# Kernel optimization log

Hardware: AMD Instinct MI355X
Metric: run time of the kernel (lower is better)

## Reference

```python
import jax, jax.numpy as jnp
import numpy as np

B, S, D, H = 2, 4096, 512, 8
HD = D // H
SCALE = float(np.sqrt(HD))


def setup_inputs() -> dict:
    key = jax.random.key(0)
    ks = jax.random.split(key, 11)
    std = 1.0 / np.sqrt(D)
    inp = {
        "query": jax.random.normal(ks[0], (B, S, D), jnp.float32),
        "key": jax.random.normal(ks[1], (B, S, D), jnp.float32),
        "value": jax.random.normal(ks[2], (B, S, D), jnp.float32),
        "Wq": jax.random.normal(ks[3], (D, D), jnp.float32) * std,
        "bq": jnp.zeros((D,), jnp.float32),
        "Wk": jax.random.normal(ks[4], (D, D), jnp.float32) * std,
        "bk": jnp.zeros((D,), jnp.float32),
        "Wv": jax.random.normal(ks[5], (D, D), jnp.float32) * std,
        "bv": jnp.zeros((D,), jnp.float32),
        "Wo": jax.random.normal(ks[6], (D, D), jnp.float32) * std,
        "bo": jnp.zeros((D,), jnp.float32),
    }
    return inp


def reference(query, key, value, Wq, bq, Wk, bk, Wv, bv, Wo, bo):
    # Linear projections, split into heads: [B, H, S, HD]
    def proj(x, W, b):
        y = jnp.einsum('bsd,df->bsf', x, W) + b
        return y.reshape(B, -1, H, HD).transpose(0, 2, 1, 3)

    Q = proj(query, Wq, bq)
    K = proj(key, Wk, bk)
    V = proj(value, Wv, bv)

    # Full [B, H, S, S] score matrix (faithful to the naive original)
    scores = jnp.einsum('bhqd,bhkd->bhqk', Q, K) / SCALE
    attn = jax.nn.softmax(scores, axis=-1)  # dropout = identity in eval
    attended = jnp.einsum('bhqk,bhkd->bhqd', attn, V)
    attended = attended.transpose(0, 2, 1, 3).reshape(B, -1, D)
    return jnp.einsum('bsd,df->bsf', attended, Wo) + bo
```

## Files before the change

kernel.cpp:

```cpp
#include <hip/hip_runtime.h>

typedef short short8 __attribute__((ext_vector_type(8)));
typedef short short4v __attribute__((ext_vector_type(4)));
typedef float f32x4 __attribute__((ext_vector_type(4)));
typedef float f32x16 __attribute__((ext_vector_type(16)));
typedef unsigned uint2v __attribute__((ext_vector_type(2)));

typedef __attribute__((address_space(1))) void gvoid;
typedef __attribute__((address_space(3))) void lvoid;

#define DEV static __device__ __forceinline__

constexpr int Dm = 512;
constexpr int Sm = 4096;
constexpr int Hh = 8;
constexpr long NTe = (long)2 * Sm * Dm;

#define QSCALE 0.18033688011112042f

DEV short f2bf(float f) {
  union { float f; unsigned u; } v; v.f = f;
  unsigned r = v.u + 0x7FFFu + ((v.u >> 16) & 1u);
  return (short)(r >> 16);
}

DEV float bf2f(short s) {
  unsigned u = ((unsigned)(unsigned short)s) << 16;
  union { unsigned u; float f; } v; v.u = u;
  return v.f;
}

DEV float exp2_fast(float x) {
#if __has_builtin(__builtin_amdgcn_exp2f)
  return __builtin_amdgcn_exp2f(x);
#else
  return exp2f(x);
#endif
}

DEV float max3f(float a, float b, float c) { return fmaxf(fmaxf(a, b), c); }

DEV unsigned cvt_pk_bf16(float lo, float hi) {
  unsigned r;
  asm("v_cvt_pk_bf16_f32 %0, %1, %2" : "=v"(r) : "v"(lo), "v"(hi));
  return r;
}

DEV int fr(int r) { return (r & 7) ^ (((r >> 3) & 1) << 2); }

DEV uint2v pl32swap(unsigned a, unsigned b) {
  return __builtin_amdgcn_permlane32_swap(a, b, false, false);
}
DEV float swap_max(float x) { return fmaxf(x, __shfl_xor(x, 32, 64)); }
DEV float swap_add(float x) { return x + __shfl_xor(x, 32, 64); }

DEV void async16(const void* g, void* l) {
  __builtin_amdgcn_global_load_lds((gvoid*)g, (lvoid*)l, 16, 0, 0);
}

__global__ __launch_bounds__(256) void cast_qkv(
    const float* __restrict__ q, const float* __restrict__ k,
    const float* __restrict__ v, short* __restrict__ xq,
    short* __restrict__ xk, short* __restrict__ xv) {
  int t = blockIdx.y;
  const float* src = (t == 0) ? q : (t == 1) ? k : v;
  short* dst = (t == 0) ? xq : (t == 1) ? xk : xv;
  long i = (long)(blockIdx.x * 256 + threadIdx.x) * 4;
  float4 f = *(const float4*)(src + i);
  short4v o;
  o[0] = f2bf(f.x); o[1] = f2bf(f.y); o[2] = f2bf(f.z); o[3] = f2bf(f.w);
  *(short4v*)(dst + i) = o;
}

__global__ __launch_bounds__(256) void wtrans(
    const float* __restrict__ wq, const float* __restrict__ wk,
    const float* __restrict__ wv, const float* __restrict__ wo,
    short* __restrict__ wt) {
  __shared__ short T[64 * 72];
  const int tid = threadIdx.x;
  const int n0 = blockIdx.x * 64, k0 = blockIdx.y * 64, w = blockIdx.z;
  const float* W = (w == 0) ? wq : (w == 1) ? wk : (w == 2) ? wv : wo;
  for (int t = 0; t < 4; ++t) {
    int flat = t * 256 + tid;
    int r = flat >> 4, c4 = flat & 15;
    float4 f = *(const float4*)(W + (k0 + r) * 512 + n0 + c4 * 4);
    T[(c4 * 4 + 0) * 72 + r] = f2bf(f.x);
    T[(c4 * 4 + 1) * 72 + r] = f2bf(f.y);
    T[(c4 * 4 + 2) * 72 + r] = f2bf(f.z);
    T[(c4 * 4 + 3) * 72 + r] = f2bf(f.w);
  }
  __syncthreads();
  for (int t = 0; t < 2; ++t) {
    int flat = t * 256 + tid;
    int r = flat >> 3, c = flat & 7;
    short8 v = *(const short8*)(T + r * 72 + c * 8);
    *(short8*)(wt + ((long)w << 18) + (n0 + r) * 512 + k0 + c * 8) = v;
  }
}

__global__ __launch_bounds__(256) void vtrans(
    const short* __restrict__ V, short* __restrict__ VT) {
  __shared__ short T[64 * 72];
  const int tid = threadIdx.x;
  const int s0 = blockIdx.x * 64, d0 = blockIdx.y * 64, b = blockIdx.z;
  for (int t = 0; t < 2; ++t) {
    int flat = t * 256 + tid;
    int sl = flat >> 3, c = flat & 7;
    short8 v = *(const short8*)(V + ((long)b * Sm + s0 + sl) * Dm + d0 + c * 8);
    for (int j = 0; j < 8; ++j) T[(c * 8 + j) * 72 + sl] = v[j];
  }
  __syncthreads();
  for (int t = 0; t < 2; ++t) {
    int flat = t * 256 + tid;
    int dl = flat >> 3, c = flat & 7;
    short8 v = *(const short8*)(T + dl * 72 + c * 8);
    *(short8*)(VT + ((long)b * Dm + d0 + dl) * Sm + s0 + c * 8) = v;
  }
}

template <bool OUT_BF16>
DEV void gemm_body(const short* __restrict__ A, const short* __restrict__ Bt,
                   const float* __restrict__ bias, float scale,
                   void* __restrict__ Yv, short* As, short* Bs) {
  constexpr int K = 512, N = 512, BK = 64;
  const int tid = threadIdx.x, lane = tid & 63, w = tid >> 6;
  const int lm = lane & 15, lg = lane >> 4;
  const int wr = w >> 1, wc = w & 1;
  const long bm = (long)blockIdx.y * 128;
  const long bn = (long)blockIdx.x * 128;
  f32x4 zero = {0.f, 0.f, 0.f, 0.f};
  f32x4 acc[4][4];
  for (int m = 0; m < 4; ++m)
    for (int n = 0; n < 4; ++n) acc[m][n] = zero;
  for (int k0 = 0; k0 < K; k0 += BK) {
    __syncthreads();
    for (int t = 0; t < 4; ++t) {
      int flat = t * 256 + tid;
      int row = flat >> 3, c = flat & 7;
      async16(A + (bm + row) * K + k0 + ((c ^ fr(row)) * 8), As + flat * 8);
    }
    for (int t = 0; t < 4; ++t) {
      int flat = t * 256 + tid;
      int row = flat >> 3, c = flat & 7;
      async16(Bt + (bn + row) * K + k0 + ((c ^ fr(row)) * 8), Bs + flat * 8);
    }
    __syncthreads();
    for (int kk = 0; kk < 2; ++kk) {
      short8 a[4], b[4];
      for (int m = 0; m < 4; ++m)
        a[m] = *(const short8*)(As + (wr * 64 + m * 16 + lm) * BK +
                                ((kk * 4 + lg) ^ fr(lm)) * 8);
      for (int n = 0; n < 4; ++n)
        b[n] = *(const short8*)(Bs + (wc * 64 + n * 16 + lm) * BK +
                                ((kk * 4 + lg) ^ fr(lm)) * 8);
      for (int m = 0; m < 4; ++m)
        for (int n = 0; n < 4; ++n)
          acc[m][n] = __builtin_amdgcn_mfma_f32_16x16x32_bf16(a[m], b[n], acc[m][n], 0, 0, 0);
    }
  }
  for (int m = 0; m < 4; ++m)
    for (int n = 0; n < 4; ++n) {
      long row0 = bm + wr * 64 + m * 16 + lg * 4;
      int col = (int)bn + wc * 64 + n * 16 + lm;
      float bb = bias[col];
      for (int j = 0; j < 4; ++j) {
        float val = (acc[m][n][j] + bb) * scale;
        if (OUT_BF16)
          ((short*)Yv)[(row0 + j) * N + col] = f2bf(val);
        else
          ((float*)Yv)[(row0 + j) * N + col] = val;
      }
    }
}

__global__ __launch_bounds__(256) void gemm_proj(
    const short* __restrict__ Xq, const short* __restrict__ Xk,
    const short* __restrict__ Xv, const short* __restrict__ Wt,
    const float* __restrict__ bq, const float* __restrict__ bk,
    const float* __restrict__ bv, short* __restrict__ Qb,
    short* __restrict__ Kb, short* __restrict__ Vb) {
  __shared__ short As[128 * 64];
  __shared__ short Bs[128 * 64];
  int z = blockIdx.z;
  const short* A = (z == 0) ? Xq : (z == 1) ? Xk : Xv;
  const short* Bt = Wt + (long)z * 512 * 512;
  const float* bias = (z == 0) ? bq : (z == 1) ? bk : bv;
  short* Y = (z == 0) ? Qb : (z == 1) ? Kb : Vb;
  float scale = (z == 0) ? QSCALE : 1.f;
  gemm_body<true>(A, Bt, bias, scale, Y, As, Bs);
}

__global__ __launch_bounds__(256) void gemm_out(
    const short* __restrict__ A, const short* __restrict__ Bt,
    const float* __restrict__ bias, float* __restrict__ Y) {
  __shared__ short As[128 * 64];
  __shared__ short Bs[128 * 64];
  gemm_body<false>(A, Bt, bias, 1.f, Y, As, Bs);
}

template <int NSPLIT>
__global__ __launch_bounds__(512) void attn(
    const short* __restrict__ Qb, const short* __restrict__ Kb,
    const short* __restrict__ VTb, short* __restrict__ Op0,
    short* __restrict__ OpRest, float2* __restrict__ Ml) {
  __shared__ short Ks[4][64 * 64];
  __shared__ short Vt[4][64 * 64];
  const int tid = threadIdx.x, lane = tid & 63, w = tid >> 6;
  const int q32 = lane & 31, l5 = lane >> 5;
  const int bh = blockIdx.y, b = bh >> 3, h = bh & 7;
  const int z = blockIdx.z;
  constexpr int KVLEN = Sm / NSPLIT;
  const int kvbase = z * KVLEN;
  const long baseQ = (long)b * Sm * Dm + h * 64;
  const long baseVT = ((long)b * Dm + h * 64) * Sm;
  const int q0w = blockIdx.x * 256 + w * 32;

  short8 qf[4];
#pragma unroll
  for (int ks = 0; ks < 4; ++ks)
    qf[ks] = *(const short8*)(Qb + baseQ + (long)(q0w + q32) * Dm + ks * 16 + l5 * 8);

  f32x16 o0, o1;
#pragma unroll
  for (int r = 0; r < 16; ++r) { o0[r] = 0.f; o1[r] = 0.f; }
  float mrun = -1e30f, lrun = 0.f;

  const int r0 = tid >> 3, c0 = tid & 7;
  const short* gk0 = Kb + baseQ + (long)(kvbase + r0) * Dm + (c0 ^ fr(r0)) * 8;
  const short* gv0 = VTb + baseVT + (long)r0 * Sm + kvbase + (c0 ^ fr(r0)) * 8;
  const int l0 = tid * 8;

  auto stage = [&](int buf) {
    async16(gk0, &Ks[buf][l0]);
    async16(gv0, &Vt[buf][l0]);
    gk0 += 64 * Dm; gv0 += 64;
  };

  stage(0);
  stage(1);
  __syncthreads();

  const int cxor = fr(q32);

  auto tile_body = [&](int buf) {
    f32x16 sc0, sc1;
#pragma unroll
    for (int r = 0; r < 16; ++r) { sc0[r] = 0.f; sc1[r] = 0.f; }
    __builtin_amdgcn_s_setprio(1);
#pragma unroll
    for (int ks = 0; ks < 4; ++ks) {
      int cx = (2 * ks + l5) ^ cxor;
      short8 kf0 = *(const short8*)(&Ks[buf][q32 * 64 + cx * 8]);
      short8 kf1 = *(const short8*)(&Ks[buf][(32 + q32) * 64 + cx * 8]);
      sc0 = __builtin_amdgcn_mfma_f32_32x32x16_bf16(kf0, qf[ks], sc0, 0, 0, 0);
      sc1 = __builtin_amdgcn_mfma_f32_32x32x16_bf16(kf1, qf[ks], sc1, 0, 0, 0);
    }
    __builtin_amdgcn_s_setprio(0);

    float t1 = max3f(sc0[0], sc0[1], sc0[2]);
    float t2 = max3f(sc0[3], sc0[4], sc0[5]);
    float t3 = max3f(sc0[6], sc0[7], sc0[8]);
    float t4 = max3f(sc0[9], sc0[10], sc0[11]);
    float t5 = max3f(sc0[12], sc0[13], sc0[14]);
    float ma = max3f(max3f(t1, t2, t3), max3f(t4, t5, sc0[15]), sc1[0]);
    t1 = max3f(sc1[1], sc1[2], sc1[3]);
    t2 = max3f(sc1[4], sc1[5], sc1[6]);
    t3 = max3f(sc1[7], sc1[8], sc1[9]);
    t4 = max3f(sc1[10], sc1[11], sc1[12]);
    t5 = max3f(sc1[13], sc1[14], sc1[15]);
    float tmax_lane = fmaxf(ma, max3f(max3f(t1, t2, t3), t4, t5));

    if (__any(tmax_lane > mrun + 8.f)) {
      float tmax = swap_max(tmax_lane);
      float mi = fmaxf(mrun, tmax);
      float cc = exp2_fast(mrun - mi);
      mrun = mi;
      lrun *= cc;
#pragma unroll
      for (int r = 0; r < 16; ++r) {
        float ccr = __shfl(cc, ((r & 3) + 8 * (r >> 2)) + 4 * l5, 32);
        o0[r] *= ccr;
        o1[r] *= ccr;
      }
    }

    float la[4] = {0.f, 0.f, 0.f, 0.f}, lb[4] = {0.f, 0.f, 0.f, 0.f};
#pragma unroll
    for (int r = 0; r < 16; ++r) {
      sc0[r] = exp2_fast(sc0[r] - mrun); la[r & 3] += sc0[r];
      sc1[r] = exp2_fast(sc1[r] - mrun); lb[r & 3] += sc1[r];
    }
    lrun += ((la[0] + la[1]) + (la[2] + la[3])) +
            ((lb[0] + lb[1]) + (lb[2] + lb[3]));

    __builtin_amdgcn_s_setprio(1);
#pragma unroll
    for (int kc = 0; kc < 4; ++kc) {
      const f32x16& sch = (kc < 2) ? sc0 : sc1;
      const int bb = 8 * (kc & 1);
      unsigned A = cvt_pk_bf16(sch[bb + 0], sch[bb + 1]);
      unsigned B = cvt_pk_bf16(sch[bb + 2], sch[bb + 3]);
      unsigned C = cvt_pk_bf16(sch[bb + 4], sch[bb + 5]);
      unsigned D = cvt_pk_bf16(sch[bb + 6], sch[bb + 7]);
      uint2v rac = pl32swap(A, C);
      uint2v rbd = pl32swap(B, D);
      union { unsigned u[4]; short8 s; } pu;
      pu.u[0] = rac[0]; pu.u[1] = rbd[0]; pu.u[2] = rac[1]; pu.u[3] = rbd[1];
      int cx = (2 * kc + l5) ^ cxor;
      short8 vf0 = *(const short8*)(&Vt[buf][q32 * 64 + cx * 8]);
      short8 vf1 = *(const short8*)(&Vt[buf][(32 + q32) * 64 + cx * 8]);
      o0 = __builtin_amdgcn_mfma_f32_32x32x16_bf16(pu.s, vf0, o0, 0, 0, 0);
      o1 = __builtin_amdgcn_mfma_f32_32x32x16_bf16(pu.s, vf1, o1, 0, 0, 0);
    }
    __builtin_amdgcn_s_setprio(0);
  };

  constexpr int NTILES = KVLEN / 64;
  for (int it = 0; it < NTILES; it += 2) {
    const int p2 = (it >> 1) & 1;
    if (it + 2 < NTILES) {
      stage(2 * (1 - p2));
      stage(2 * (1 - p2) + 1);
    }
    tile_body(2 * p2);
    tile_body(2 * p2 + 1);
    __syncthreads();
  }

  lrun = swap_add(lrun);

  short* Op = (z == 0) ? Op0 : OpRest + (long)(z - 1) * NTe;
#pragma unroll
  for (int r = 0; r < 16; ++r) {
    int q = (r & 3) + 8 * (r >> 2) + 4 * l5;
    long rowoff = baseQ + (long)(q0w + q) * Dm;
    Op[rowoff + q32] = f2bf(o0[r]);
    Op[rowoff + 32 + q32] = f2bf(o1[r]);
  }
  if (l5 == 0) {
    float2 ml; ml.x = mrun; ml.y = lrun;
    Ml[(long)(z * 16 + bh) * Sm + q0w + q32] = ml;
  }
}

template <int NSPLIT>
__global__ __launch_bounds__(256) void mergeN(
    const short* __restrict__ Op0, const short* __restrict__ OpRest,
    const float2* __restrict__ Ml, short* __restrict__ Ob) {
  long idx = (long)blockIdx.x * 256 + threadIdx.x;
  long row = idx >> 6;
  int c8 = (int)(idx & 63);
  int col = c8 * 8;
  int h = col >> 6;
  int b = (int)(row >> 12);
  int s = (int)(row & 4095);
  int bh = b * 8 + h;
  float2 ml[NSPLIT];
  float M = -3e38f;
#pragma unroll
  for (int z = 0; z < NSPLIT; ++z) {
    ml[z] = Ml[(long)(z * 16 + bh) * Sm + s];
    M = fmaxf(M, ml[z].x);
  }
  float wz[NSPLIT], den = 0.f;
#pragma unroll
  for (int z = 0; z < NSPLIT; ++z) {
    wz[z] = exp2_fast(ml[z].x - M);
    den += ml[z].y * wz[z];
  }
  float inv = 1.0f / den;
  long off = row * 512 + col;
  float acc[8];
#pragma unroll
  for (int i = 0; i < 8; ++i) acc[i] = 0.f;
#pragma unroll
  for (int z = 0; z < NSPLIT; ++z) {
    const short* Op = (z == 0) ? Op0 : OpRest + (long)(z - 1) * NTe;
    short8 v = *(const short8*)(Op + off);
#pragma unroll
    for (int i = 0; i < 8; ++i) acc[i] += bf2f(v[i]) * wz[z];
  }
  short8 o;
#pragma unroll
  for (int i = 0; i < 8; ++i) o[i] = f2bf(acc[i] * inv);
  *(short8*)(Ob + off) = o;
}

extern "C" void kernel_launch(void* const* d_in, const int* in_sizes, int n_in,
                              void* d_out, int out_size, void* d_ws, size_t ws_size,
                              hipStream_t stream) {
  const float* query = (const float*)d_in[0];
  const float* key_  = (const float*)d_in[1];
  const float* value = (const float*)d_in[2];
  const float* Wq = (const float*)d_in[3]; const float* bq = (const float*)d_in[4];
  const float* Wk = (const float*)d_in[5]; const float* bk = (const float*)d_in[6];
  const float* Wv = (const float*)d_in[7]; const float* bv = (const float*)d_in[8];
  const float* Wo = (const float*)d_in[9]; const float* bo = (const float*)d_in[10];

  short* Xq = (short*)d_ws;
  short* Xk = Xq + NTe;
  short* Xv = Xk + NTe;
  short* Wt = Xv + NTe;
  short* Qb = Wt + 4 * 512 * 512;
  short* Kb = Qb + NTe;
  short* Vb = Kb + NTe;
  short* VT = Xv;
  short* Op0 = Xq;
  short* OpRest = Vb + NTe;
  short* Ob = Vb;

  const size_t base_bytes = (size_t)(6 * NTe + 4 * 512 * 512) * 2;
  const size_t need4 = base_bytes + 3 * (size_t)NTe * 2 + (size_t)4 * 16 * Sm * 8;
  const int nsplit = (ws_size >= need4) ? 4 : 2;
  float2* Ml = (float2*)(OpRest + (size_t)(nsplit - 1) * NTe);

  cast_qkv<<<dim3(4096, 3), 256, 0, stream>>>(query, key_, value, Xq, Xk, Xv);
  wtrans<<<dim3(8, 8, 4), 256, 0, stream>>>(Wq, Wk, Wv, Wo, Wt);

  gemm_proj<<<dim3(4, 64, 3), 256, 0, stream>>>(Xq, Xk, Xv, Wt, bq, bk, bv,
                                                Qb, Kb, Vb);

  vtrans<<<dim3(Sm / 64, Dm / 64, 2), 256, 0, stream>>>(Vb, VT);

  if (nsplit == 4) {
    attn<4><<<dim3(Sm / 256, 2 * Hh, 4), 512, 0, stream>>>(Qb, Kb, VT, Op0,
                                                           OpRest, Ml);
    mergeN<4><<<dim3((2 * Sm * 512 / 8) / 256), 256, 0, stream>>>(Op0, OpRest,
                                                                  Ml, Ob);
  } else {
    attn<2><<<dim3(Sm / 256, 2 * Hh, 2), 512, 0, stream>>>(Qb, Kb, VT, Op0,
                                                           OpRest, Ml);
    mergeN<2><<<dim3((2 * Sm * 512 / 8) / 256), 256, 0, stream>>>(Op0, OpRest,
                                                                  Ml, Ob);
  }

  gemm_out<<<dim3(4, 64), 256, 0, stream>>>(Ob, Wt + 3L * 512 * 512, bo,
                                            (float*)d_out);
}
```

Before: 157.1 us.

## Compute softmax row sums with MFMA against ones and fix split-KV at two

The per-lane VALU accumulation of the softmax denominator is replaced by an extra MFMA that multiplies the bf16 probabilities by a vector of ones, so the row sum accumulates in matrix-core registers alongside the output. The rescale path now also scales this sum accumulator, and the final per-row sum is written from the MFMA layout. The host also drops the runtime choice of a 4-way KV split and always launches the 2-way split and merge. This adds a third MFMA per step and 16 accumulator registers, and the sum now uses bf16-rounded probabilities, which slightly changes numerics.

Measured after the change: 161.5 us. 1.03x slower.

```diff
diff --git a/kernel.cpp b/kernel.cpp
--- a/kernel.cpp
+++ b/kernel.cpp
@@ -52,7 +52,6 @@
   return __builtin_amdgcn_permlane32_swap(a, b, false, false);
 }
 DEV float swap_max(float x) { return fmaxf(x, __shfl_xor(x, 32, 64)); }
-DEV float swap_add(float x) { return x + __shfl_xor(x, 32, 64); }
 
 DEV void async16(const void* g, void* l) {
   __builtin_amdgcn_global_load_lds((gvoid*)g, (lvoid*)l, 16, 0, 0);
@@ -220,10 +219,14 @@
   for (int ks = 0; ks < 4; ++ks)
     qf[ks] = *(const short8*)(Qb + baseQ + (long)(q0w + q32) * Dm + ks * 16 + l5 * 8);
 
-  f32x16 o0, o1;
-#pragma unroll
-  for (int r = 0; r < 16; ++r) { o0[r] = 0.f; o1[r] = 0.f; }
-  float mrun = -1e30f, lrun = 0.f;
+  short8 vones;
+#pragma unroll
+  for (int j = 0; j < 8; ++j) vones[j] = (short)0x3F80;
+
+  f32x16 o0, o1, lacc;
+#pragma unroll
+  for (int r = 0; r < 16; ++r) { o0[r] = 0.f; o1[r] = 0.f; lacc[r] = 0.f; }
+  float mrun = -1e30f;
 
   const int r0 = tid >> 3, c0 = tid & 7;
   const short* gk0 = Kb + baseQ + (long)(kvbase + r0) * Dm + (c0 ^ fr(r0)) * 8;
@@ -275,23 +278,20 @@
       float mi = fmaxf(mrun, tmax);
       float cc = exp2_fast(mrun - mi);
       mrun = mi;
-      lrun *= cc;
 #pragma unroll
       for (int r = 0; r < 16; ++r) {
         float ccr = __shfl(cc, ((r & 3) + 8 * (r >> 2)) + 4 * l5, 32);
         o0[r] *= ccr;
         o1[r] *= ccr;
+        lacc[r] *= ccr;
       }
     }
 
-    float la[4] = {0.f, 0.f, 0.f, 0.f}, lb[4] = {0.f, 0.f, 0.f, 0.f};
 #pragma unroll
     for (int r = 0; r < 16; ++r) {
-      sc0[r] = exp2_fast(sc0[r] - mrun); la[r & 3] += sc0[r];
-      sc1[r] = exp2_fast(sc1[r] - mrun); lb[r & 3] += sc1[r];
-    }
-    lrun += ((la[0] + la[1]) + (la[2] + la[3])) +
-            ((lb[0] + lb[1]) + (lb[2] + lb[3]));
+      sc0[r] = exp2_fast(sc0[r] - mrun);
+      sc1[r] = exp2_fast(sc1[r] - mrun);
+    }
 
     __builtin_amdgcn_s_setprio(1);
 #pragma unroll
@@ -311,6 +311,7 @@
       short8 vf1 = *(const short8*)(&Vt[buf][(32 + q32) * 64 + cx * 8]);
       o0 = __builtin_amdgcn_mfma_f32_32x32x16_bf16(pu.s, vf0, o0, 0, 0, 0);
       o1 = __builtin_amdgcn_mfma_f32_32x32x16_bf16(pu.s, vf1, o1, 0, 0, 0);
+      lacc = __builtin_amdgcn_mfma_f32_32x32x16_bf16(pu.s, vones, lacc, 0, 0, 0);
     }
     __builtin_amdgcn_s_setprio(0);
   };
@@ -327,8 +328,6 @@
     __syncthreads();
   }
 
-  lrun = swap_add(lrun);
-
   short* Op = (z == 0) ? Op0 : OpRest + (long)(z - 1) * NTe;
 #pragma unroll
   for (int r = 0; r < 16; ++r) {
@@ -337,9 +336,15 @@
     Op[rowoff + q32] = f2bf(o0[r]);
     Op[rowoff + 32 + q32] = f2bf(o1[r]);
   }
-  if (l5 == 0) {
-    float2 ml; ml.x = mrun; ml.y = lrun;
-    Ml[(long)(z * 16 + bh) * Sm + q0w + q32] = ml;
+  const long mlbase = (long)(z * 16 + bh) * Sm + q0w;
+  if (l5 == 0)
+    Ml[mlbase + q32].x = mrun;
+  if (q32 == 0) {
+#pragma unroll
+    for (int r = 0; r < 16; ++r) {
+      int q = (r & 3) + 8 * (r >> 2) + 4 * l5;
+      Ml[mlbase + q].y = lacc[r];
+    }
   }
 }
 
@@ -408,11 +413,7 @@
   short* Op0 = Xq;
   short* OpRest = Vb + NTe;
   short* Ob = Vb;
-
-  const size_t base_bytes = (size_t)(6 * NTe + 4 * 512 * 512) * 2;
-  const size_t need4 = base_bytes + 3 * (size_t)NTe * 2 + (size_t)4 * 16 * Sm * 8;
-  const int nsplit = (ws_size >= need4) ? 4 : 2;
-  float2* Ml = (float2*)(OpRest + (size_t)(nsplit - 1) * NTe);
+  float2* Ml = (float2*)(OpRest + NTe);
 
   cast_qkv<<<dim3(4096, 3), 256, 0, stream>>>(query, key_, value, Xq, Xk, Xv);
   wtrans<<<dim3(8, 8, 4), 256, 0, stream>>>(Wq, Wk, Wv, Wo, Wt);
@@ -422,17 +423,10 @@
 
   vtrans<<<dim3(Sm / 64, Dm / 64, 2), 256, 0, stream>>>(Vb, VT);
 
-  if (nsplit == 4) {
-    attn<4><<<dim3(Sm / 256, 2 * Hh, 4), 512, 0, stream>>>(Qb, Kb, VT, Op0,
-                                                           OpRest, Ml);
-    mergeN<4><<<dim3((2 * Sm * 512 / 8) / 256), 256, 0, stream>>>(Op0, OpRest,
-                                                                  Ml, Ob);
-  } else {
-    attn<2><<<dim3(Sm / 256, 2 * Hh, 2), 512, 0, stream>>>(Qb, Kb, VT, Op0,
-                                                           OpRest, Ml);
-    mergeN<2><<<dim3((2 * Sm * 512 / 8) / 256), 256, 0, stream>>>(Op0, OpRest,
-                                                                  Ml, Ob);
-  }
+  attn<2><<<dim3(Sm / 256, 2 * Hh, 2), 512, 0, stream>>>(Qb, Kb, VT, Op0,
+                                                         OpRest, Ml);
+  mergeN<2><<<dim3((2 * Sm * 512 / 8) / 256), 256, 0, stream>>>(Op0, OpRest,
+                                                                Ml, Ob);
 
   gemm_out<<<dim3(4, 64), 256, 0, stream>>>(Ob, Wt + 3L * 512 * 512, bo,
                                             (float*)d_out);
```
